# Optimization experiments

Measured on AMD Instinct MI355X. Metric: run time of the kernel, lower is better.

The kernel has to match this reference:

```python
import jax, jax.numpy as jnp
import numpy as np

BLOCK = 512
WINDOW = 2
NEG = -1e9


def _pad_to_block(x, block):
    pad_len = (-x.shape[1]) % block
    if pad_len:
        x = jnp.pad(x, ((0, 0), (0, pad_len), (0, 0)))
    return x


def setup_inputs() -> dict:
    key = jax.random.key(0)
    ks = jax.random.split(key, 8)
    B, Lq, Lk, C = 2, 8192, 8192, 128
    s = 1.0 / np.sqrt(C)
    return {
        "query": jax.random.normal(ks[0], (B, Lq, C), jnp.float32),
        "key_value": jax.random.normal(ks[1], (B, Lk, C), jnp.float32),
        "Wq": jax.random.normal(ks[2], (C, C), jnp.float32) * s,
        "bq": jax.random.normal(ks[3], (C,), jnp.float32) * 0.01,
        "Wkv": jax.random.normal(ks[4], (C, 2 * C), jnp.float32) * s,
        "bkv": jax.random.normal(ks[5], (2 * C,), jnp.float32) * 0.01,
        "Wo": jax.random.normal(ks[6], (C, C), jnp.float32) * s,
        "bo": jax.random.normal(ks[7], (C,), jnp.float32) * 0.01,
    }


def reference(query, key_value, Wq, bq, Wkv, bkv, Wo, bo):
    B, Lq, C = query.shape
    qp = _pad_to_block(query, BLOCK)
    kp = _pad_to_block(key_value, BLOCK)
    q = qp @ Wq + bq                      # [B, Lq_pad, C]
    kv = kp @ Wkv + bkv                   # [B, Lk_pad, 2C]
    k, v = kv[..., :C], kv[..., C:]
    nq = qp.shape[1] // BLOCK
    nk = kp.shape[1] // BLOCK
    qb = q.reshape(B, nq, BLOCK, C)
    kb = k.reshape(B, nk, BLOCK, C)
    vb = v.reshape(B, nk, BLOCK, C)
    allowed = jnp.abs(jnp.arange(nq)[:, None] - jnp.arange(nk)[None, :]) <= WINDOW  # [nq, nk]
    # scores: [B, nq, nk, s, d] with s = q-pos in block, d = k-pos in block
    scores = jnp.einsum('bqsc,bkdc->bqksd', qb, kb) / jnp.sqrt(jnp.asarray(C, qb.dtype))
    scores = jnp.where(allowed[None, :, :, None, None], scores, NEG)
    # NOTE: faithful to original torch code, softmax over axis=3 (the 's' axis)
    attn = jax.nn.softmax(scores, axis=3)
    out = jnp.einsum('bqksd,bkdc->bqsc', attn, vb)
    out = out.reshape(B, nq * BLOCK, C)[:, :Lq]
    return out @ Wo + bo
```

## Files before the change

### kernel.cpp

```cpp
#include <hip/hip_runtime.h>

typedef _Float16 f16;
typedef _Float16 half8 __attribute__((ext_vector_type(8)));
typedef float floatx4 __attribute__((ext_vector_type(4)));

#define MFMA16(a,b,c) __builtin_amdgcn_mfma_f32_16x16x32_f16((a),(b),(c),0,0,0)
#define RSL2E 0.12751743f

__device__ __forceinline__ void split2(float x, f16 &h, f16 &l) {
  f16 hh = (f16)x;
  h = hh;
  l = (f16)(x - (float)hh);
}

__device__ __forceinline__ void stage_rows64(const f16* __restrict__ g, int gstride,
                                             f16* lds, int rows, int tid, int nthr) {
  int total = rows * 8;
  for (int idx = tid; idx < total; idx += nthr) {
    int row = idx >> 3, slot = idx & 7;
    float4 v = *(const float4*)(g + (size_t)row * gstride + slot * 8);
    int lofs = ((row << 7) + (slot << 4)) ^ ((row & 7) << 4);
    *(float4*)((char*)lds + lofs) = v;
  }
}
__device__ __forceinline__ void stage_rows128(const f16* __restrict__ g, int gstride,
                                              f16* lds, int rows, int tid, int nthr) {
  int total = rows * 16;
  for (int idx = tid; idx < total; idx += nthr) {
    int row = idx >> 4, slot = idx & 15;
    float4 v = *(const float4*)(g + (size_t)row * gstride + slot * 8);
    int lofs = ((row << 8) + (slot << 4)) ^ ((row & 7) << 4);
    *(float4*)((char*)lds + lofs) = v;
  }
}
__device__ __forceinline__ void stage_split64(const float* __restrict__ g, int gstride,
                                              f16* ldsh, f16* ldsl, int rows,
                                              int tid, int nthr) {
  int total = rows * 16;
  for (int idx = tid; idx < total; idx += nthr) {
    int row = idx >> 4, cg = idx & 15;
    float4 va = *(const float4*)(g + (size_t)row * gstride + cg * 4);
    union { f16 a[4]; uint2 u; } hh, ll;
    split2(va.x, hh.a[0], ll.a[0]);
    split2(va.y, hh.a[1], ll.a[1]);
    split2(va.z, hh.a[2], ll.a[2]);
    split2(va.w, hh.a[3], ll.a[3]);
    int lofs = ((row << 7) + (cg << 3)) ^ ((row & 7) << 4);
    *(uint2*)((char*)ldsh + lofs) = hh.u;
    *(uint2*)((char*)ldsl + lofs) = ll.u;
  }
}
__device__ __forceinline__ half8 fragP128(const f16* lds, int row, int kofs) {
  int ofs = ((row << 7) + (kofs << 1)) ^ ((row & 7) << 4);
  return *(const half8*)((const char*)lds + ofs);
}
__device__ __forceinline__ half8 fragP256(const f16* lds, int row, int kofs) {
  int ofs = ((row << 8) + (kofs << 1)) ^ ((row & 7) << 4);
  return *(const half8*)((const char*)lds + ofs);
}

__global__ void k_splitW(const float* __restrict__ Wq, const float* __restrict__ Wkv,
                         const float* __restrict__ Wo,
                         f16* WqTh, f16* WqTl, f16* WkvTh, f16* WkvTl,
                         f16* WoTh, f16* WoTl) {
  int idx = blockIdx.x * 256 + threadIdx.x;
  if (idx >= 65536) return;
  float v; f16 *ph, *pl; int dst;
  if (idx < 16384) {
    int n = idx >> 7, c = idx & 127;
    v = Wq[c * 128 + n]; ph = WqTh; pl = WqTl; dst = idx;
  } else if (idx < 49152) {
    int t = idx - 16384; int n = t >> 7, c = t & 127;
    v = Wkv[c * 256 + n]; ph = WkvTh; pl = WkvTl; dst = t;
  } else {
    int t = idx - 49152; int n = t >> 7, c = t & 127;
    v = Wo[c * 128 + n]; ph = WoTh; pl = WoTl; dst = t;
  }
  f16 h, l; split2(v, h, l);
  ph[dst] = h; pl[dst] = l;
}

__global__ __launch_bounds__(512, 2)
void k_proj(const float* __restrict__ query, const float* __restrict__ key_value,
            const f16* __restrict__ WqTh, const f16* __restrict__ WqTl,
            const f16* __restrict__ WkvTh, const f16* __restrict__ WkvTl,
            const float* __restrict__ bq, const float* __restrict__ bkv,
            f16* __restrict__ qhp, f16* __restrict__ khp, f16* __restrict__ vT) {
  int pidx = blockIdx.x >> 8, blk = blockIdx.x & 255;
  const float* A; const f16 *BTh, *BTl; const float* bias; f16* out; int mode;
  if (pidx == 0)      { A = query;     BTh = WqTh;          BTl = WqTl;          bias = bq;        out = qhp; mode = 0; }
  else if (pidx == 1) { A = key_value; BTh = WkvTh;         BTl = WkvTl;         bias = bkv;       out = khp; mode = 0; }
  else                { A = key_value; BTh = WkvTh + 16384; BTl = WkvTl + 16384; bias = bkv + 128; out = vT;  mode = 1; }
  __shared__ f16 pool[24576];
  f16* sAh = pool;
  f16* sAl = pool + 4096;
  f16* sBh = pool + 8192;
  f16* sBl = pool + 16384;
  int tid = threadIdx.x, wave = tid >> 6, lane = tid & 63, lg = lane >> 4, lr = lane & 15;
  int wm = wave >> 2, wn = wave & 3;
  size_t rowbase = (size_t)blk * 64;
  floatx4 zero = {0.f, 0.f, 0.f, 0.f};
  floatx4 acc[2][2] = {{zero, zero}, {zero, zero}};
  for (int cc = 0; cc < 128; cc += 64) {
    __syncthreads();
    stage_split64(A + rowbase * 128 + cc, 128, sAh, sAl, 64, tid, 512);
    stage_rows64(BTh + cc, 128, sBh, 128, tid, 512);
    stage_rows64(BTl + cc, 128, sBl, 128, tid, 512);
    __syncthreads();
    for (int kc = 0; kc < 64; kc += 32) {
      half8 ah[2], al[2];
      for (int fm = 0; fm < 2; fm++) {
        ah[fm] = fragP128(sAh, wm * 32 + fm * 16 + lr, kc + lg * 8);
        al[fm] = fragP128(sAl, wm * 32 + fm * 16 + lr, kc + lg * 8);
      }
      for (int fn = 0; fn < 2; fn++) {
        half8 bh = fragP128(sBh, wn * 32 + fn * 16 + lr, kc + lg * 8);
        half8 bl = fragP128(sBl, wn * 32 + fn * 16 + lr, kc + lg * 8);
        for (int fm = 0; fm < 2; fm++) {
          acc[fm][fn] = MFMA16(ah[fm], bh, acc[fm][fn]);
          acc[fm][fn] = MFMA16(ah[fm], bl, acc[fm][fn]);
          acc[fm][fn] = MFMA16(al[fm], bh, acc[fm][fn]);
        }
      }
    }
  }
  __syncthreads();
  f16* e = pool;
  for (int fm = 0; fm < 2; fm++) for (int fn = 0; fn < 2; fn++) {
    int n = wn * 32 + fn * 16 + lr;
    float bs = bias[n];
    for (int jj = 0; jj < 4; jj++) {
      int m = wm * 32 + fm * 16 + lg * 4 + jj;
      e[m * 136 + n] = (f16)(acc[fm][fn][jj] + bs);
    }
  }
  __syncthreads();
  if (mode == 0) {
    for (int idx = tid; idx < 1024; idx += 512) {
      int r = idx >> 4, sl = idx & 15;
      *(float4*)(out + (rowbase + r) * 128 + sl * 8) =
          *(const float4*)((const char*)e + r * 272 + sl * 16);
    }
  } else {
    size_t bidx = rowbase >> 13, lofs = rowbase & 8191;
    for (int idx = tid; idx < 1024; idx += 512) {
      int c = idx >> 3, sl = idx & 7;
      union { f16 a[8]; float4 v; } th;
      for (int t = 0; t < 8; t++) th.a[t] = e[(sl * 8 + t) * 136 + c];
      *(float4*)(out + (bidx * 128 + c) * 8192 + lofs + sl * 8) = th.v;
    }
  }
}

__global__ __launch_bounds__(512, 2)
void k_final(const float* __restrict__ Pbuf, const float* __restrict__ U,
             const f16* __restrict__ BTh, const f16* __restrict__ BTl,
             const float* __restrict__ bias, float* __restrict__ out) {
  __shared__ f16 pool[24576];
  f16* sAh = pool;
  f16* sAl = pool + 4096;
  f16* sBh = pool + 8192;
  f16* sBl = pool + 16384;
  int tid = threadIdx.x, wave = tid >> 6, lane = tid & 63, lg = lane >> 4, lr = lane & 15;
  int wm = wave >> 2, wn = wave & 3;
  size_t rowbase = (size_t)blockIdx.x * 64;
  int b = (int)(rowbase >> 13), r0 = (int)(rowbase & 8191);
  int i = r0 >> 9, st = (r0 >> 6) & 7;
  const float* p0 = Pbuf + ((size_t)(((b * 16 + i) * 8 + st) * 4)) * 8192;
  const float* p1 = p0 + 8192;
  const float* p2 = p0 + 16384;
  const float* p3 = p0 + 24576;
  const float* Ub = U + ((size_t)b * 16 + i) * 128;
  floatx4 zero = {0.f, 0.f, 0.f, 0.f};
  floatx4 acc[2][2] = {{zero, zero}, {zero, zero}};
  for (int cc = 0; cc < 128; cc += 64) {
    __syncthreads();
    for (int idx = tid; idx < 1024; idx += 512) {
      int row = idx >> 4, cg = idx & 15;
      int c = cc + cg * 4;
      float4 a0 = *(const float4*)(p0 + row * 128 + c);
      float4 a1 = *(const float4*)(p1 + row * 128 + c);
      float4 a2 = *(const float4*)(p2 + row * 128 + c);
      float4 a3 = *(const float4*)(p3 + row * 128 + c);
      float4 uu = *(const float4*)(Ub + c);
      float vals[4] = {(a0.x + a1.x) + (a2.x + a3.x) + uu.x,
                       (a0.y + a1.y) + (a2.y + a3.y) + uu.y,
                       (a0.z + a1.z) + (a2.z + a3.z) + uu.z,
                       (a0.w + a1.w) + (a2.w + a3.w) + uu.w};
      union { f16 a[4]; uint2 u; } hh, ll;
      for (int t = 0; t < 4; t++) split2(vals[t], hh.a[t], ll.a[t]);
      int lofs = ((row << 7) + (cg << 3)) ^ ((row & 7) << 4);
      *(uint2*)((char*)sAh + lofs) = hh.u;
      *(uint2*)((char*)sAl + lofs) = ll.u;
    }
    stage_rows64(BTh + cc, 128, sBh, 128, tid, 512);
    stage_rows64(BTl + cc, 128, sBl, 128, tid, 512);
    __syncthreads();
    for (int kc = 0; kc < 64; kc += 32) {
      half8 ah[2], al[2];
      for (int fm = 0; fm < 2; fm++) {
        ah[fm] = fragP128(sAh, wm * 32 + fm * 16 + lr, kc + lg * 8);
        al[fm] = fragP128(sAl, wm * 32 + fm * 16 + lr, kc + lg * 8);
      }
      for (int fn = 0; fn < 2; fn++) {
        half8 bh = fragP128(sBh, wn * 32 + fn * 16 + lr, kc + lg * 8);
        half8 bl = fragP128(sBl, wn * 32 + fn * 16 + lr, kc + lg * 8);
        for (int fm = 0; fm < 2; fm++) {
          acc[fm][fn] = MFMA16(ah[fm], bh, acc[fm][fn]);
          acc[fm][fn] = MFMA16(ah[fm], bl, acc[fm][fn]);
          acc[fm][fn] = MFMA16(al[fm], bh, acc[fm][fn]);
        }
      }
    }
  }
  __syncthreads();
  float* ef = (float*)pool;
  for (int fm = 0; fm < 2; fm++) for (int fn = 0; fn < 2; fn++) {
    int n = wn * 32 + fn * 16 + lr;
    float bs = bias[n];
    for (int jj = 0; jj < 4; jj++) {
      int m = wm * 32 + fm * 16 + lg * 4 + jj;
      ef[m * 132 + n] = acc[fm][fn][jj] + bs;
    }
  }
  __syncthreads();
  for (int idx = tid; idx < 2048; idx += 512) {
    int r = idx >> 5, sl = idx & 31;
    *(float4*)(out + (rowbase + r) * 128 + sl * 4) = *(const float4*)(ef + r * 132 + sl * 4);
  }
}

__global__ void k_U(const f16* __restrict__ vT, float* __restrict__ U) {
  int b = blockIdx.x >> 7, c = blockIdx.x & 127;
  int tid = threadIdx.x;
  const f16* r = vT + ((size_t)b * 128 + c) * 8192;
  float s = 0.f;
  const float4* r4 = (const float4*)(r + tid * 32);
  for (int t = 0; t < 4; t++) {
    float4 v = r4[t];
    const f16* a = (const f16*)&v;
    for (int u = 0; u < 8; u++) s += (float)a[u];
  }
  __shared__ float part[256];
  __shared__ float bs[16];
  part[tid] = s;
  __syncthreads();
  if (tid < 16) {
    float t = 0.f;
    for (int u = 0; u < 16; u++) t += part[tid * 16 + u];
    bs[tid] = t;
  }
  __syncthreads();
  if (tid < 16) {
    int i = tid;
    float tot = 0.f;
    for (int j = 0; j < 16; j++) tot += bs[j];
    int j0 = i - 2 < 0 ? 0 : i - 2;
    int j1 = i + 2 > 15 ? 15 : i + 2;
    float win = 0.f;
    for (int j = j0; j <= j1; j++) win += bs[j];
    U[((size_t)b * 16 + i) * 128 + c] = (tot - win) * (1.0f / 512.0f);
  }
}

__global__ __launch_bounds__(512, 4)
void k_passA(const f16* __restrict__ kp, const f16* __restrict__ qp,
             float* __restrict__ Z) {
  int bid = blockIdx.x;
  int wg = (bid & 7) * 80 + (bid >> 3);
  int dchunk = wg & 3; int rest = wg >> 2;
  int slot = rest % 5; int rest2 = rest / 5;
  int i = rest2 & 15; int b = rest2 >> 4;
  int j = i - 2 + slot;
  if (j < 0 || j > 15) return;
  __shared__ f16 sK[16384], sQ[16384];
  int tid = threadIdx.x, wave = tid >> 6, lane = tid & 63, lg = lane >> 4, lr = lane & 15;
  int wm = wave >> 1, wn = wave & 1;
  size_t krow = (size_t)b * 8192 + j * 512 + dchunk * 128;
  stage_rows128(kp + krow * 128, 128, sK, 128, tid, 512);
  float zp[2][4] = {{0.f,0.f,0.f,0.f},{0.f,0.f,0.f,0.f}};
  floatx4 zero = {0.f, 0.f, 0.f, 0.f};
  for (int sc = 0; sc < 4; sc++) {
    __syncthreads();
    size_t qrow = (size_t)b * 8192 + i * 512 + sc * 128;
    stage_rows128(qp + qrow * 128, 128, sQ, 128, tid, 512);
    __syncthreads();
    floatx4 acc[2][4] = {{zero,zero,zero,zero},{zero,zero,zero,zero}};
    for (int kc = 0; kc < 128; kc += 32) {
      half8 ah[2];
      for (int fm = 0; fm < 2; fm++)
        ah[fm] = fragP256(sK, wm * 32 + fm * 16 + lr, kc + lg * 8);
      for (int fn = 0; fn < 4; fn++) {
        half8 bh = fragP256(sQ, wn * 64 + fn * 16 + lr, kc + lg * 8);
        for (int fm = 0; fm < 2; fm++)
          acc[fm][fn] = MFMA16(ah[fm], bh, acc[fm][fn]);
      }
    }
    for (int fm = 0; fm < 2; fm++) for (int fn = 0; fn < 4; fn++)
      for (int jj = 0; jj < 4; jj++)
        zp[fm][jj] += exp2f(acc[fm][fn][jj] * RSL2E);
  }
  for (int off = 1; off < 16; off <<= 1)
    for (int fm = 0; fm < 2; fm++) for (int jj = 0; jj < 4; jj++)
      zp[fm][jj] += __shfl_xor(zp[fm][jj], off, 64);
  __syncthreads();
  float* sred = (float*)sQ;
  if (lr == 0) {
    for (int fm = 0; fm < 2; fm++) for (int jj = 0; jj < 4; jj++) {
      int d = wm * 32 + fm * 16 + lg * 4 + jj;
      sred[wn * 128 + d] = zp[fm][jj];
    }
  }
  __syncthreads();
  if (tid < 128) {
    size_t zb = (((size_t)(b * 16 + i) * 16 + j) * 512) + dchunk * 128;
    Z[zb + tid] = sred[tid] + sred[128 + tid];
  }
}

__global__ __launch_bounds__(512, 4)
void k_passB(const f16* __restrict__ qp, const f16* __restrict__ kp,
             const f16* __restrict__ vT,
             const float* __restrict__ Z, float* __restrict__ Pbuf) {
  int bid = blockIdx.x;
  int wg = ((bid & 7) << 7) | (bid >> 3);
  int dq = wg & 3, st = (wg >> 2) & 7, i = (wg >> 5) & 15, b = wg >> 9;
  __shared__ __align__(16) char pool[65536];
  f16* sQ  = (f16*)pool;
  f16* sKV = (f16*)(pool + 16384);
  f16* sE  = (f16*)(pool + 49152);
  int tid = threadIdx.x, wave = tid >> 6, lane = tid & 63, lg = lane >> 4, lr = lane & 15;
  int w1m = wave >> 1, w1n = wave & 1;
  int w2m = wave >> 2, w2n = wave & 3;
  int srow = tid >> 4, sslot = tid & 15;
  int sl0 = (((srow      ) << 8) + (sslot << 4)) ^ ((srow & 7) << 4);
  int sl1 = (((srow +  32) << 8) + (sslot << 4)) ^ ((srow & 7) << 4);
  int sl2 = (((srow +  64) << 8) + (sslot << 4)) ^ ((srow & 7) << 4);
  int sl3 = (((srow +  96) << 8) + (sslot << 4)) ^ ((srow & 7) << 4);
  size_t qrow = (size_t)b * 8192 + i * 512 + st * 64;
  stage_rows128(qp + qrow * 128, 128, sQ, 64, tid, 512);
  floatx4 zero = {0.f, 0.f, 0.f, 0.f};
  floatx4 acc2[2][2] = {{zero, zero}, {zero, zero}};
  const f16* vbase = vT + (size_t)b * 1048576;
  for (int slot = 0; slot < 5; slot++) {
    int j = i - 2 + slot;
    if (j < 0 || j > 15) continue;
    const f16* kb = kp + ((size_t)b * 8192 + j * 512 + dq * 128) * 128;
    float4 k0 = *(const float4*)(kb + (size_t)(srow      ) * 128 + sslot * 8);
    float4 k1 = *(const float4*)(kb + (size_t)(srow +  32) * 128 + sslot * 8);
    float4 k2 = *(const float4*)(kb + (size_t)(srow +  64) * 128 + sslot * 8);
    float4 k3 = *(const float4*)(kb + (size_t)(srow +  96) * 128 + sslot * 8);
    const f16* gv = vbase + (size_t)j * 512 + dq * 128;
    float4 v0 = *(const float4*)(gv + (size_t)(srow      ) * 8192 + sslot * 8);
    float4 v1 = *(const float4*)(gv + (size_t)(srow +  32) * 8192 + sslot * 8);
    float4 v2 = *(const float4*)(gv + (size_t)(srow +  64) * 8192 + sslot * 8);
    float4 v3 = *(const float4*)(gv + (size_t)(srow +  96) * 8192 + sslot * 8);
    float rz[2][4];
    {
      size_t zb = (((size_t)(b * 16 + i) * 16 + j) * 512) + dq * 128;
      #pragma unroll
      for (int fm = 0; fm < 2; fm++)
        #pragma unroll
        for (int jj = 0; jj < 4; jj++)
          rz[fm][jj] = 1.0f / Z[zb + w1m * 32 + fm * 16 + lg * 4 + jj];
    }
    __syncthreads();
    *(float4*)((char*)sKV + sl0) = k0;
    *(float4*)((char*)sKV + sl1) = k1;
    *(float4*)((char*)sKV + sl2) = k2;
    *(float4*)((char*)sKV + sl3) = k3;
    __syncthreads();
    floatx4 acc1[2][2] = {{zero, zero}, {zero, zero}};
    #pragma unroll
    for (int kc = 0; kc < 128; kc += 32) {
      half8 ah0 = fragP256(sKV, w1m * 32 + lr, kc + lg * 8);
      half8 ah1 = fragP256(sKV, w1m * 32 + 16 + lr, kc + lg * 8);
      #pragma unroll
      for (int fn = 0; fn < 2; fn++) {
        half8 bq = fragP256(sQ, w1n * 32 + fn * 16 + lr, kc + lg * 8);
        acc1[0][fn] = MFMA16(ah0, bq, acc1[0][fn]);
        acc1[1][fn] = MFMA16(ah1, bq, acc1[1][fn]);
      }
    }
    __syncthreads();
    #pragma unroll
    for (int fm = 0; fm < 2; fm++)
      #pragma unroll
      for (int fn = 0; fn < 2; fn++) {
        int s = w1n * 32 + fn * 16 + lr;
        int d0 = w1m * 32 + fm * 16 + lg * 4;
        union { f16 a[4]; float2 u; } pk;
        #pragma unroll
        for (int jj = 0; jj < 4; jj++)
          pk.a[jj] = (f16)(exp2f(acc1[fm][fn][jj] * RSL2E) * rz[fm][jj]);
        int ofs = ((s << 8) + (d0 << 1)) ^ ((s & 7) << 4);
        *(float2*)((char*)sE + ofs) = pk.u;
      }
    *(float4*)((char*)sKV + sl0) = v0;
    *(float4*)((char*)sKV + sl1) = v1;
    *(float4*)((char*)sKV + sl2) = v2;
    *(float4*)((char*)sKV + sl3) = v3;
    __syncthreads();
    #pragma unroll
    for (int kc = 0; kc < 128; kc += 32) {
      half8 ea0 = fragP256(sE, w2m * 32 + lr, kc + lg * 8);
      half8 ea1 = fragP256(sE, w2m * 32 + 16 + lr, kc + lg * 8);
      #pragma unroll
      for (int fn = 0; fn < 2; fn++) {
        half8 bh = fragP256(sKV, w2n * 32 + fn * 16 + lr, kc + lg * 8);
        acc2[0][fn] = MFMA16(ea0, bh, acc2[0][fn]);
        acc2[1][fn] = MFMA16(ea1, bh, acc2[1][fn]);
      }
    }
  }
  __syncthreads();
  float* ef = (float*)pool;
  for (int fm = 0; fm < 2; fm++) for (int fn = 0; fn < 2; fn++) {
    int c = w2n * 32 + fn * 16 + lr;
    for (int jj = 0; jj < 4; jj++) {
      int s = w2m * 32 + fm * 16 + lg * 4 + jj;
      ef[s * 128 + c] = acc2[fm][fn][jj];
    }
  }
  __syncthreads();
  float* po = Pbuf + ((size_t)((((b * 16 + i) * 8 + st) * 4) + dq)) * 8192;
  for (int idx = tid; idx < 2048; idx += 512)
    ((float4*)po)[idx] = ((const float4*)ef)[idx];
}

extern "C" void kernel_launch(void* const* d_in, const int* in_sizes, int n_in,
                              void* d_out, int out_size, void* d_ws, size_t ws_size,
                              hipStream_t stream) {
  const float* query     = (const float*)d_in[0];
  const float* key_value = (const float*)d_in[1];
  const float* Wq  = (const float*)d_in[2];
  const float* bq  = (const float*)d_in[3];
  const float* Wkv = (const float*)d_in[4];
  const float* bkv = (const float*)d_in[5];
  const float* Wo  = (const float*)d_in[6];
  const float* bo  = (const float*)d_in[7];
  float* out = (float*)d_out;

  char* ws = (char*)d_ws;
  size_t off = 0;
  auto alloc = [&](size_t bytes) -> char* {
    char* p = ws + off;
    off += (bytes + 255) & ~(size_t)255;
    return p;
  };
  const size_t SZH = (size_t)16384 * 128 * 2;
  f16* qhp  = (f16*)alloc(SZH);
  f16* khp  = (f16*)alloc(SZH);
  f16* vT   = (f16*)alloc(SZH);
  float* Pbuf = (float*)alloc((size_t)1024 * 8192 * 4);
  f16* WqTh  = (f16*)alloc(32768); f16* WqTl  = (f16*)alloc(32768);
  f16* WkvTh = (f16*)alloc(65536); f16* WkvTl = (f16*)alloc(65536);
  f16* WoTh  = (f16*)alloc(32768); f16* WoTl  = (f16*)alloc(32768);
  float* Zb = (float*)alloc((size_t)2 * 16 * 16 * 512 * 4);
  float* Ub = (float*)alloc((size_t)2 * 16 * 128 * 4);
  if (off > ws_size) return;

  k_splitW<<<256, 256, 0, stream>>>(Wq, Wkv, Wo, WqTh, WqTl, WkvTh, WkvTl, WoTh, WoTl);
  k_proj<<<768, 512, 0, stream>>>(query, key_value, WqTh, WqTl, WkvTh, WkvTl,
                                  bq, bkv, qhp, khp, vT);
  k_U<<<256, 256, 0, stream>>>(vT, Ub);
  k_passA<<<640, 512, 0, stream>>>(khp, qhp, Zb);
  k_passB<<<1024, 512, 0, stream>>>(qhp, khp, vT, Zb, Pbuf);
  k_final<<<256, 512, 0, stream>>>(Pbuf, Ub, WoTh, WoTl, bo, out);
}
```

Measured before the change: 112.3 us.

## Register-prefetch next global tile during MFMA compute in proj, final, passA

Replaces the synchronous global-to-LDS staging loops in k_proj, k_final and k_passA with register double-buffering. Each thread loads its fixed slice of the next chunk into registers right after the barrier, so the global load latency overlaps the MFMA loop on the current chunk. It also unrolls the chunk loops and precomputes the swizzled LDS offsets. In exchange it raises register pressure, which could lower occupancy in these launch-bounded kernels.

```diff
diff --git a/kernel.cpp b/kernel.cpp
--- a/kernel.cpp
+++ b/kernel.cpp
@@ -33,23 +33,6 @@
     *(float4*)((char*)lds + lofs) = v;
   }
 }
-__device__ __forceinline__ void stage_split64(const float* __restrict__ g, int gstride,
-                                              f16* ldsh, f16* ldsl, int rows,
-                                              int tid, int nthr) {
-  int total = rows * 16;
-  for (int idx = tid; idx < total; idx += nthr) {
-    int row = idx >> 4, cg = idx & 15;
-    float4 va = *(const float4*)(g + (size_t)row * gstride + cg * 4);
-    union { f16 a[4]; uint2 u; } hh, ll;
-    split2(va.x, hh.a[0], ll.a[0]);
-    split2(va.y, hh.a[1], ll.a[1]);
-    split2(va.z, hh.a[2], ll.a[2]);
-    split2(va.w, hh.a[3], ll.a[3]);
-    int lofs = ((row << 7) + (cg << 3)) ^ ((row & 7) << 4);
-    *(uint2*)((char*)ldsh + lofs) = hh.u;
-    *(uint2*)((char*)ldsl + lofs) = ll.u;
-  }
-}
 __device__ __forceinline__ half8 fragP128(const f16* lds, int row, int kofs) {
   int ofs = ((row << 7) + (kofs << 1)) ^ ((row & 7) << 4);
   return *(const half8*)((const char*)lds + ofs);
@@ -57,6 +40,14 @@
 __device__ __forceinline__ half8 fragP256(const f16* lds, int row, int kofs) {
   int ofs = ((row << 8) + (kofs << 1)) ^ ((row & 7) << 4);
   return *(const half8*)((const char*)lds + ofs);
+}
+__device__ __forceinline__ void pack_split(float4 v, uint2 &h, uint2 &l) {
+  union { f16 a[4]; uint2 u; } hh, ll;
+  split2(v.x, hh.a[0], ll.a[0]);
+  split2(v.y, hh.a[1], ll.a[1]);
+  split2(v.z, hh.a[2], ll.a[2]);
+  split2(v.w, hh.a[3], ll.a[3]);
+  h = hh.u; l = ll.u;
 }
 
 __global__ void k_splitW(const float* __restrict__ Wq, const float* __restrict__ Wkv,
@@ -99,14 +90,45 @@
   int tid = threadIdx.x, wave = tid >> 6, lane = tid & 63, lg = lane >> 4, lr = lane & 15;
   int wm = wave >> 2, wn = wave & 3;
   size_t rowbase = (size_t)blk * 64;
+  int arow = tid >> 4, acg = tid & 15;
+  int al0 = ((arow << 7) + (acg << 3)) ^ ((arow & 7) << 4);
+  int al1 = (((arow + 32) << 7) + (acg << 3)) ^ ((arow & 7) << 4);
+  int brow = tid >> 3, bslot = tid & 7;
+  int bl0 = ((brow << 7) + (bslot << 4)) ^ ((brow & 7) << 4);
+  int bl1 = (((brow + 64) << 7) + (bslot << 4)) ^ ((brow & 7) << 4);
+  const float* Ab = A + rowbase * 128;
+  float4 a0 = *(const float4*)(Ab + (size_t)arow * 128 + acg * 4);
+  float4 a1 = *(const float4*)(Ab + (size_t)(arow + 32) * 128 + acg * 4);
+  float4 b0h = *(const float4*)(BTh + brow * 128 + bslot * 8);
+  float4 b1h = *(const float4*)(BTh + (brow + 64) * 128 + bslot * 8);
+  float4 b0l = *(const float4*)(BTl + brow * 128 + bslot * 8);
+  float4 b1l = *(const float4*)(BTl + (brow + 64) * 128 + bslot * 8);
   floatx4 zero = {0.f, 0.f, 0.f, 0.f};
   floatx4 acc[2][2] = {{zero, zero}, {zero, zero}};
+  #pragma unroll
   for (int cc = 0; cc < 128; cc += 64) {
     __syncthreads();
-    stage_split64(A + rowbase * 128 + cc, 128, sAh, sAl, 64, tid, 512);
-    stage_rows64(BTh + cc, 128, sBh, 128, tid, 512);
-    stage_rows64(BTl + cc, 128, sBl, 128, tid, 512);
-    __syncthreads();
+    {
+      uint2 h, l;
+      pack_split(a0, h, l);
+      *(uint2*)((char*)sAh + al0) = h; *(uint2*)((char*)sAl + al0) = l;
+      pack_split(a1, h, l);
+      *(uint2*)((char*)sAh + al1) = h; *(uint2*)((char*)sAl + al1) = l;
+    }
+    *(float4*)((char*)sBh + bl0) = b0h;
+    *(float4*)((char*)sBh + bl1) = b1h;
+    *(float4*)((char*)sBl + bl0) = b0l;
+    *(float4*)((char*)sBl + bl1) = b1l;
+    __syncthreads();
+    if (cc == 0) {
+      a0 = *(const float4*)(Ab + (size_t)arow * 128 + 64 + acg * 4);
+      a1 = *(const float4*)(Ab + (size_t)(arow + 32) * 128 + 64 + acg * 4);
+      b0h = *(const float4*)(BTh + 64 + brow * 128 + bslot * 8);
+      b1h = *(const float4*)(BTh + 64 + (brow + 64) * 128 + bslot * 8);
+      b0l = *(const float4*)(BTl + 64 + brow * 128 + bslot * 8);
+      b1l = *(const float4*)(BTl + 64 + (brow + 64) * 128 + bslot * 8);
+    }
+    #pragma unroll
     for (int kc = 0; kc < 64; kc += 32) {
       half8 ah[2], al[2];
       for (int fm = 0; fm < 2; fm++) {
@@ -171,31 +193,69 @@
   const float* p2 = p0 + 16384;
   const float* p3 = p0 + 24576;
   const float* Ub = U + ((size_t)b * 16 + i) * 128;
+  int arow = tid >> 4, acg = tid & 15;
+  int al0 = ((arow << 7) + (acg << 3)) ^ ((arow & 7) << 4);
+  int al1 = (((arow + 32) << 7) + (acg << 3)) ^ ((arow & 7) << 4);
+  int brow = tid >> 3, bslot = tid & 7;
+  int bl0 = ((brow << 7) + (bslot << 4)) ^ ((brow & 7) << 4);
+  int bl1 = (((brow + 64) << 7) + (bslot << 4)) ^ ((brow & 7) << 4);
+  int c0 = acg * 4;
+  float4 r0a0 = *(const float4*)(p0 + arow * 128 + c0);
+  float4 r0a1 = *(const float4*)(p1 + arow * 128 + c0);
+  float4 r0a2 = *(const float4*)(p2 + arow * 128 + c0);
+  float4 r0a3 = *(const float4*)(p3 + arow * 128 + c0);
+  float4 r1a0 = *(const float4*)(p0 + (arow + 32) * 128 + c0);
+  float4 r1a1 = *(const float4*)(p1 + (arow + 32) * 128 + c0);
+  float4 r1a2 = *(const float4*)(p2 + (arow + 32) * 128 + c0);
+  float4 r1a3 = *(const float4*)(p3 + (arow + 32) * 128 + c0);
+  float4 uu = *(const float4*)(Ub + c0);
+  float4 b0h = *(const float4*)(BTh + brow * 128 + bslot * 8);
+  float4 b1h = *(const float4*)(BTh + (brow + 64) * 128 + bslot * 8);
+  float4 b0l = *(const float4*)(BTl + brow * 128 + bslot * 8);
+  float4 b1l = *(const float4*)(BTl + (brow + 64) * 128 + bslot * 8);
   floatx4 zero = {0.f, 0.f, 0.f, 0.f};
   floatx4 acc[2][2] = {{zero, zero}, {zero, zero}};
+  #pragma unroll
   for (int cc = 0; cc < 128; cc += 64) {
     __syncthreads();
-    for (int idx = tid; idx < 1024; idx += 512) {
-      int row = idx >> 4, cg = idx & 15;
-      int c = cc + cg * 4;
-      float4 a0 = *(const float4*)(p0 + row * 128 + c);
-      float4 a1 = *(const float4*)(p1 + row * 128 + c);
-      float4 a2 = *(const float4*)(p2 + row * 128 + c);
-      float4 a3 = *(const float4*)(p3 + row * 128 + c);
-      float4 uu = *(const float4*)(Ub + c);
-      float vals[4] = {(a0.x + a1.x) + (a2.x + a3.x) + uu.x,
-                       (a0.y + a1.y) + (a2.y + a3.y) + uu.y,
-                       (a0.z + a1.z) + (a2.z + a3.z) + uu.z,
-                       (a0.w + a1.w) + (a2.w + a3.w) + uu.w};
-      union { f16 a[4]; uint2 u; } hh, ll;
-      for (int t = 0; t < 4; t++) split2(vals[t], hh.a[t], ll.a[t]);
-      int lofs = ((row << 7) + (cg << 3)) ^ ((row & 7) << 4);
-      *(uint2*)((char*)sAh + lofs) = hh.u;
-      *(uint2*)((char*)sAl + lofs) = ll.u;
-    }
-    stage_rows64(BTh + cc, 128, sBh, 128, tid, 512);
-    stage_rows64(BTl + cc, 128, sBl, 128, tid, 512);
-    __syncthreads();
+    {
+      float4 s0, s1;
+      s0.x = (r0a0.x + r0a1.x) + (r0a2.x + r0a3.x) + uu.x;
+      s0.y = (r0a0.y + r0a1.y) + (r0a2.y + r0a3.y) + uu.y;
+      s0.z = (r0a0.z + r0a1.z) + (r0a2.z + r0a3.z) + uu.z;
+      s0.w = (r0a0.w + r0a1.w) + (r0a2.w + r0a3.w) + uu.w;
+      s1.x = (r1a0.x + r1a1.x) + (r1a2.x + r1a3.x) + uu.x;
+      s1.y = (r1a0.y + r1a1.y) + (r1a2.y + r1a3.y) + uu.y;
+      s1.z = (r1a0.z + r1a1.z) + (r1a2.z + r1a3.z) + uu.z;
+      s1.w = (r1a0.w + r1a1.w) + (r1a2.w + r1a3.w) + uu.w;
+      uint2 h, l;
+      pack_split(s0, h, l);
+      *(uint2*)((char*)sAh + al0) = h; *(uint2*)((char*)sAl + al0) = l;
+      pack_split(s1, h, l);
+      *(uint2*)((char*)sAh + al1) = h; *(uint2*)((char*)sAl + al1) = l;
+    }
+    *(float4*)((char*)sBh + bl0) = b0h;
+    *(float4*)((char*)sBh + bl1) = b1h;
+    *(float4*)((char*)sBl + bl0) = b0l;
+    *(float4*)((char*)sBl + bl1) = b1l;
+    __syncthreads();
+    if (cc == 0) {
+      int c1 = 64 + acg * 4;
+      r0a0 = *(const float4*)(p0 + arow * 128 + c1);
+      r0a1 = *(const float4*)(p1 + arow * 128 + c1);
+      r0a2 = *(const float4*)(p2 + arow * 128 + c1);
+      r0a3 = *(const float4*)(p3 + arow * 128 + c1);
+      r1a0 = *(const float4*)(p0 + (arow + 32) * 128 + c1);
+      r1a1 = *(const float4*)(p1 + (arow + 32) * 128 + c1);
+      r1a2 = *(const float4*)(p2 + (arow + 32) * 128 + c1);
+      r1a3 = *(const float4*)(p3 + (arow + 32) * 128 + c1);
+      uu   = *(const float4*)(Ub + c1);
+      b0h = *(const float4*)(BTh + 64 + brow * 128 + bslot * 8);
+      b1h = *(const float4*)(BTh + 64 + (brow + 64) * 128 + bslot * 8);
+      b0l = *(const float4*)(BTl + 64 + brow * 128 + bslot * 8);
+      b1l = *(const float4*)(BTl + 64 + (brow + 64) * 128 + bslot * 8);
+    }
+    #pragma unroll
     for (int kc = 0; kc < 64; kc += 32) {
       half8 ah[2], al[2];
       for (int fm = 0; fm < 2; fm++) {
@@ -278,13 +338,32 @@
   int wm = wave >> 1, wn = wave & 1;
   size_t krow = (size_t)b * 8192 + j * 512 + dchunk * 128;
   stage_rows128(kp + krow * 128, 128, sK, 128, tid, 512);
+  int qr = tid >> 4, qsl = tid & 15;
+  int ql0 = ((qr << 8) + (qsl << 4)) ^ ((qr & 7) << 4);
+  int ql1 = (((qr + 32) << 8) + (qsl << 4)) ^ ((qr & 7) << 4);
+  int ql2 = (((qr + 64) << 8) + (qsl << 4)) ^ ((qr & 7) << 4);
+  int ql3 = (((qr + 96) << 8) + (qsl << 4)) ^ ((qr & 7) << 4);
+  const f16* qb = qp + ((size_t)b * 8192 + i * 512) * 128;
+  float4 q0 = *(const float4*)(qb + (size_t)(qr      ) * 128 + qsl * 8);
+  float4 q1 = *(const float4*)(qb + (size_t)(qr +  32) * 128 + qsl * 8);
+  float4 q2 = *(const float4*)(qb + (size_t)(qr +  64) * 128 + qsl * 8);
+  float4 q3 = *(const float4*)(qb + (size_t)(qr +  96) * 128 + qsl * 8);
   float zp[2][4] = {{0.f,0.f,0.f,0.f},{0.f,0.f,0.f,0.f}};
   floatx4 zero = {0.f, 0.f, 0.f, 0.f};
   for (int sc = 0; sc < 4; sc++) {
     __syncthreads();
-    size_t qrow = (size_t)b * 8192 + i * 512 + sc * 128;
-    stage_rows128(qp + qrow * 128, 128, sQ, 128, tid, 512);
-    __syncthreads();
+    *(float4*)((char*)sQ + ql0) = q0;
+    *(float4*)((char*)sQ + ql1) = q1;
+    *(float4*)((char*)sQ + ql2) = q2;
+    *(float4*)((char*)sQ + ql3) = q3;
+    __syncthreads();
+    if (sc < 3) {
+      const f16* qn = qb + (size_t)(sc + 1) * 128 * 128;
+      q0 = *(const float4*)(qn + (size_t)(qr      ) * 128 + qsl * 8);
+      q1 = *(const float4*)(qn + (size_t)(qr +  32) * 128 + qsl * 8);
+      q2 = *(const float4*)(qn + (size_t)(qr +  64) * 128 + qsl * 8);
+      q3 = *(const float4*)(qn + (size_t)(qr +  96) * 128 + qsl * 8);
+    }
     floatx4 acc[2][4] = {{zero,zero,zero,zero},{zero,zero,zero,zero}};
     for (int kc = 0; kc < 128; kc += 32) {
       half8 ah[2];
```

Result: faster. 106.1 us (median of 2 runs) (-5.5%).
